# Kernel tuning notes

Measured on AMD Instinct MI355X. Metric: run time of the kernel, lower is better.

Reference implementation:

```python
import jax, jax.numpy as jnp
import numpy as np

B, T_ENC, IN, H, SEQ_OUT = 1024, 50, 99, 2112, 25


def _lstm_cell(x, h, c, W_ih, b_ih, W_hh, b_hh):
    # gates: [B, 4H], torch LSTMCell gate order is i, f, g, o
    gates = x @ W_ih.T + b_ih + h @ W_hh.T + b_hh
    i, f, g, o = jnp.split(gates, 4, axis=-1)
    c_new = jax.nn.sigmoid(f) * c + jax.nn.sigmoid(i) * jnp.tanh(g)
    h_new = jax.nn.sigmoid(o) * jnp.tanh(c_new)
    return h_new, c_new


def setup_inputs() -> dict:
    key = jax.random.key(0)
    ks = jax.random.split(key, 14)
    s = 0.04
    return {
        "hidden_states": jax.random.normal(ks[0], (B, T_ENC, H), jnp.float32),
        "cell_states": jax.random.normal(ks[1], (B, T_ENC, H), jnp.float32),
        "global_t_state": jax.random.normal(ks[2], (B, H), jnp.float32),
        "p": jax.random.normal(ks[3], (B, 1, IN), jnp.float32),
        "W_ih0": jax.random.normal(ks[4], (4 * H, IN), jnp.float32) * s,
        "b_ih0": jax.random.normal(ks[5], (4 * H,), jnp.float32) * s,
        "W_hh0": jax.random.normal(ks[6], (4 * H, H), jnp.float32) * s,
        "b_hh0": jax.random.normal(ks[7], (4 * H,), jnp.float32) * s,
        "W_ih1": jax.random.normal(ks[8], (4 * H, H), jnp.float32) * s,
        "b_ih1": jax.random.normal(ks[9], (4 * H,), jnp.float32) * s,
        "W_hh1": jax.random.normal(ks[10], (4 * H, H), jnp.float32) * s,
        "b_hh1": jax.random.normal(ks[11], (4 * H,), jnp.float32) * s,
        "W_out": jax.random.normal(ks[12], (H, IN), jnp.float32) * s,
        "b_out": jax.random.normal(ks[13], (IN,), jnp.float32) * s,
    }


def reference(hidden_states, cell_states, global_t_state, p,
              W_ih0, b_ih0, W_hh0, b_hh0,
              W_ih1, b_ih1, W_hh1, b_hh1,
              W_out, b_out):
    # initial states: layer 0 uses mean over encoder hidden states,
    # layer 1 uses mean over [global_t_state ; hidden_states]
    h0 = hidden_states.mean(axis=1)                                   # [B, H]
    h1 = jnp.concatenate((global_t_state[:, None, :], hidden_states), axis=1).mean(axis=1)
    c0 = cell_states.mean(axis=1)
    c1 = c0
    pre0 = p[:, 0, :]                                                 # seed input [B, IN]

    def step(carry, _):
        h0, c0, h1, c1, prev = carry
        h0n, c0n = _lstm_cell(prev, h0, c0, W_ih0, b_ih0, W_hh0, b_hh0)
        h1n, c1n = _lstm_cell(h0n, h1, c1, W_ih1, b_ih1, W_hh1, b_hh1)
        pre = h1n @ W_out + b_out + prev                              # residual on cell-0 input
        return (h0n, c0n, h1n, c1n, pre), pre

    _, pres = jax.lax.scan(step, (h0, c0, h1, c1, pre0), None, length=SEQ_OUT)
    return pres.transpose(1, 0, 2)                                    # [B, SEQ_OUT, IN]
```

## Files before the change

kernel.cpp:

```cpp
#include <hip/hip_runtime.h>

#define B_    1024
#define H_    2112
#define FH    8448
#define IN_   99
#define TENC  50
#define SEQ   25
#define K0    2240
#define K1    4224
#define LDX0  2240
#define LDX1  4224
#define KT0   35
#define KT1   66
#define HB_   132

typedef __bf16 bf16;
typedef __bf16 bf16x8 __attribute__((ext_vector_type(8)));
typedef __bf16 bf16x4 __attribute__((ext_vector_type(4)));
typedef float  f32x4  __attribute__((ext_vector_type(4)));

__device__ __forceinline__ void gload_lds16(const void* g, void* l) {
  __builtin_amdgcn_global_load_lds(
      (const __attribute__((address_space(1))) void*)g,
      (__attribute__((address_space(3))) void*)l, 16, 0, 0);
}

__device__ __forceinline__ float sigf(float x) { return 1.f / (1.f + __expf(-x)); }
__device__ __forceinline__ float tanhfast(float x) { return 1.f - 2.f / (__expf(2.f * x) + 1.f); }

__global__ __launch_bounds__(128, 3)
void lstm_gemm_cell(const bf16* __restrict__ X, int lda, int K,
                    const bf16* __restrict__ Wpk,
                    const float* __restrict__ bsum,
                    float* __restrict__ Cst,
                    bf16* __restrict__ d1, int ld1,
                    bf16* __restrict__ d2, int ld2)
{
  __shared__ __align__(16) bf16 As[128 * 64];

  const int vid = (blockIdx.x & 7) * 132 + (blockIdx.x >> 3);
  const int hb  = vid >> 3;
  const int hc0 = hb * 16;
  const int m0  = (vid & 7) * 128;

  const int tid  = threadIdx.x;
  const int srow = tid >> 3;
  const int scol = ((tid & 7) ^ (srow & 7)) * 8;

  const bf16* Ab = X + (size_t)(m0 + srow) * lda + scol;

  const int lane = tid & 63;
  const int w    = tid >> 6;
  const int lr   = lane & 15, lq = lane >> 4;
  const int xs   = lr & 7;
  const int cof0 = (lq ^ xs) * 8;
  const int cof1 = ((4 + lq) ^ xs) * 8;

  const int KT = K >> 6;
  const bf16* Wp = Wpk + (size_t)hb * KT * 4096 + lane * 8;

  f32x4 acc[4][4];
#pragma unroll
  for (int a = 0; a < 4; ++a)
#pragma unroll
    for (int b = 0; b < 4; ++b) acc[a][b] = (f32x4){0.f, 0.f, 0.f, 0.f};

  for (int kt = 0; kt < KT; ++kt) {
    const int ko = kt * 64;
#pragma unroll
    for (int it = 0; it < 8; ++it)
      gload_lds16(Ab + (size_t)it * 16 * lda + ko, &As[it * 1024 + tid * 8]);

    const bf16* Wt = Wp + (size_t)kt * 4096;
    bf16x8 bfr[4][2];
#pragma unroll
    for (int nf = 0; nf < 4; ++nf) {
      bfr[nf][0] = *(const bf16x8*)&Wt[(nf * 2 + 0) * 512];
      bfr[nf][1] = *(const bf16x8*)&Wt[(nf * 2 + 1) * 512];
    }
    __syncthreads();

    bf16x8 af[4][2];
#pragma unroll
    for (int mi = 0; mi < 4; ++mi) {
      const int r = (w * 64 + mi * 16 + lr) * 64;
      af[mi][0] = *(const bf16x8*)&As[r + cof0];
      af[mi][1] = *(const bf16x8*)&As[r + cof1];
    }
#pragma unroll
    for (int mi = 0; mi < 4; ++mi)
#pragma unroll
      for (int nf = 0; nf < 4; ++nf)
#pragma unroll
        for (int kc = 0; kc < 2; ++kc)
          acc[mi][nf] = __builtin_amdgcn_mfma_f32_16x16x32_bf16(
              af[mi][kc], bfr[nf][kc], acc[mi][nf], 0, 0, 0);
    __syncthreads();
  }

  const int hc = hc0 + lr;
  const float bi  = bsum[hc];
  const float bff = bsum[H_ + hc];
  const float bg  = bsum[2 * H_ + hc];
  const float bo  = bsum[3 * H_ + hc];

#pragma unroll
  for (int mi = 0; mi < 4; ++mi) {
#pragma unroll
    for (int r = 0; r < 4; ++r) {
      const int m = m0 + w * 64 + mi * 16 + lq * 4 + r;
      const float gi = acc[mi][0][r] + bi;
      const float gf = acc[mi][1][r] + bff;
      const float gg = acc[mi][2][r] + bg;
      const float go = acc[mi][3][r] + bo;
      const size_t ci = (size_t)m * H_ + hc;
      const float c_old = Cst[ci];
      const float cn = sigf(gf) * c_old + sigf(gi) * tanhfast(gg);
      const float hn = sigf(go) * tanhfast(cn);
      Cst[ci] = cn;
      const bf16 hb2 = (bf16)hn;
      d1[(size_t)m * ld1 + hc] = hb2;
      if (d2) d2[(size_t)m * ld2 + hc] = hb2;
    }
  }
}

__global__ __launch_bounds__(256, 1)
void out_gemm(const bf16* __restrict__ Hin,
              const bf16* __restrict__ Wo,
              const float* __restrict__ b_out,
              float* __restrict__ prev,
              bf16* __restrict__ X0n,
              float* __restrict__ out, int t)
{
  __shared__ float red[4][4][112];
  const int tid = threadIdx.x;
  const int m0 = blockIdx.x * 4;
  const int lane = tid & 63, wv = tid >> 6;
  const int lr = lane & 15, lq = lane >> 4, lk = lq * 8;

  f32x4 acc[7];
#pragma unroll
  for (int b = 0; b < 7; ++b) acc[b] = (f32x4){0.f, 0.f, 0.f, 0.f};

  const int start = (wv == 0) ? 0 : (1 + wv * 8);
  const int cnt = (wv == 0) ? 9 : 8;

  for (int kt = start; kt < start + cnt; ++kt) {
    const int ko = kt * 64;
    bf16x8 av[2], bv[7][2];
#pragma unroll
    for (int kc = 0; kc < 2; ++kc)
      av[kc] = *(const bf16x8*)&Hin[(size_t)(m0 + (lr & 3)) * LDX1 + ko + kc * 32 + lk];
#pragma unroll
    for (int nf = 0; nf < 7; ++nf)
#pragma unroll
      for (int kc = 0; kc < 2; ++kc)
        bv[nf][kc] = *(const bf16x8*)&Wo[(size_t)(nf * 16 + lr) * H_ + ko + kc * 32 + lk];
#pragma unroll
    for (int nf = 0; nf < 7; ++nf)
#pragma unroll
      for (int kc = 0; kc < 2; ++kc)
        acc[nf] = __builtin_amdgcn_mfma_f32_16x16x32_bf16(av[kc], bv[nf][kc], acc[nf], 0, 0, 0);
  }

  if (lq == 0) {
#pragma unroll
    for (int nf = 0; nf < 7; ++nf)
#pragma unroll
      for (int r = 0; r < 4; ++r)
        red[wv][r][nf * 16 + lr] = acc[nf][r];
  }
  __syncthreads();

  for (int idx = tid; idx < 4 * 112; idx += 256) {
    const int ml = idx / 112, n = idx - ml * 112;
    if (n < IN_) {
      const int m = m0 + ml;
      float s = red[0][ml][n] + red[1][ml][n] + red[2][ml][n] + red[3][ml][n] + b_out[n];
      const float pre = s + prev[m * 112 + n];
      prev[m * 112 + n] = pre;
      out[((size_t)m * SEQ + t) * IN_ + n] = pre;
      X0n[(size_t)m * LDX0 + n] = (bf16)pre;
    }
  }
}

__global__ void init_state(const float* __restrict__ hs, const float* __restrict__ cs,
                           const float* __restrict__ gts,
                           bf16* __restrict__ X0a, bf16* __restrict__ X1a,
                           float* __restrict__ c0, float* __restrict__ c1)
{
  const int h4 = blockIdx.x * 256 + threadIdx.x;
  if (h4 >= 528) return;
  const int b = blockIdx.y;
  const float4* hp = (const float4*)(hs + (size_t)b * TENC * H_) + h4;
  const float4* cp = (const float4*)(cs + (size_t)b * TENC * H_) + h4;
  float4 sh = {0.f, 0.f, 0.f, 0.f}, sc = {0.f, 0.f, 0.f, 0.f};
  for (int tt = 0; tt < TENC; ++tt) {
    float4 a = hp[tt * 528];
    sh.x += a.x; sh.y += a.y; sh.z += a.z; sh.w += a.w;
    float4 c = cp[tt * 528];
    sc.x += c.x; sc.y += c.y; sc.z += c.z; sc.w += c.w;
  }
  const float4 g = ((const float4*)(gts + (size_t)b * H_))[h4];
  const float4 c0v = {sc.x / 50.f, sc.y / 50.f, sc.z / 50.f, sc.w / 50.f};
  ((float4*)(c0 + (size_t)b * H_))[h4] = c0v;
  ((float4*)(c1 + (size_t)b * H_))[h4] = c0v;
  bf16x4 h0b = {(bf16)(sh.x / 50.f), (bf16)(sh.y / 50.f), (bf16)(sh.z / 50.f), (bf16)(sh.w / 50.f)};
  *(bf16x4*)&X0a[(size_t)b * LDX0 + 128 + h4 * 4] = h0b;
  bf16x4 h1b = {(bf16)((sh.x + g.x) / 51.f), (bf16)((sh.y + g.y) / 51.f),
                (bf16)((sh.z + g.z) / 51.f), (bf16)((sh.w + g.w) / 51.f)};
  *(bf16x4*)&X1a[(size_t)b * LDX1 + 2112 + h4 * 4] = h1b;
}

__global__ void init_prev(const float* __restrict__ p, float* __restrict__ prev,
                          bf16* __restrict__ X0a, bf16* __restrict__ X0b)
{
  const int idx = blockIdx.x * 256 + threadIdx.x;
  const int b = idx >> 7, n = idx & 127;
  const float v = (n < IN_) ? p[(size_t)b * IN_ + n] : 0.f;
  if (n < 112) prev[b * 112 + n] = v;
  X0a[(size_t)b * LDX0 + n] = (bf16)v;
  X0b[(size_t)b * LDX0 + n] = (bf16)0.f;
}

__global__ void pack_w0_frag(const float* __restrict__ Wih, const float* __restrict__ Whh,
                             bf16* __restrict__ Wpk)
{
  const int kt = blockIdx.x, hb = blockIdx.y;
  const int lane = threadIdx.x;
  const int lr = lane & 15, lq = lane >> 4;
  bf16* dst = Wpk + (((size_t)hb * KT0 + kt) * 8) * 512 + lane * 8;
#pragma unroll
  for (int fi = 0; fi < 8; ++fi) {
    const int nf = fi >> 1, kc = fi & 1;
    const int row = nf * H_ + hb * 16 + lr;
    const int k0 = kt * 64 + kc * 32 + lq * 8;
    bf16x8 v;
#pragma unroll
    for (int e = 0; e < 8; ++e) {
      const int k = k0 + e;
      float f;
      if (k < IN_)        f = Wih[(size_t)row * IN_ + k];
      else if (k < 128)   f = 0.f;
      else                f = Whh[(size_t)row * H_ + (k - 128)];
      v[e] = (bf16)f;
    }
    *(bf16x8*)(dst + fi * 512) = v;
  }
}

__global__ void pack_w1_frag(const float* __restrict__ Wih, const float* __restrict__ Whh,
                             bf16* __restrict__ Wpk)
{
  const int kt = blockIdx.x, hb = blockIdx.y;
  const int lane = threadIdx.x;
  const int lr = lane & 15, lq = lane >> 4;
  bf16* dst = Wpk + (((size_t)hb * KT1 + kt) * 8) * 512 + lane * 8;
#pragma unroll
  for (int fi = 0; fi < 8; ++fi) {
    const int nf = fi >> 1, kc = fi & 1;
    const int row = nf * H_ + hb * 16 + lr;
    const int k0 = kt * 64 + kc * 32 + lq * 8;
    bf16x8 v;
#pragma unroll
    for (int e = 0; e < 8; ++e) {
      const int k = k0 + e;
      const float f = (k < H_) ? Wih[(size_t)row * H_ + k]
                               : Whh[(size_t)row * H_ + (k - H_)];
      v[e] = (bf16)f;
    }
    *(bf16x8*)(dst + fi * 512) = v;
  }
}

__global__ void pack_wo(const float* __restrict__ W, bf16* __restrict__ Wo)
{
  const int n = blockIdx.x;
  for (int k = threadIdx.x; k < H_; k += 256)
    Wo[(size_t)n * H_ + k] = (n < IN_) ? (bf16)W[(size_t)k * IN_ + n] : (bf16)0.f;
}

__global__ void pack_bias(const float* __restrict__ bi0, const float* __restrict__ bh0,
                          const float* __restrict__ bi1, const float* __restrict__ bh1,
                          float* __restrict__ bs0, float* __restrict__ bs1)
{
  const int i = blockIdx.x * 256 + threadIdx.x;
  if (i < FH) { bs0[i] = bi0[i] + bh0[i]; bs1[i] = bi1[i] + bh1[i]; }
}

extern "C" void kernel_launch(void* const* d_in, const int* in_sizes, int n_in,
                              void* d_out, int out_size, void* d_ws, size_t ws_size,
                              hipStream_t stream)
{
  (void)in_sizes; (void)n_in; (void)out_size; (void)ws_size;
  const float* hs   = (const float*)d_in[0];
  const float* cs   = (const float*)d_in[1];
  const float* gts  = (const float*)d_in[2];
  const float* p    = (const float*)d_in[3];
  const float* Wih0 = (const float*)d_in[4];
  const float* bih0 = (const float*)d_in[5];
  const float* Whh0 = (const float*)d_in[6];
  const float* bhh0 = (const float*)d_in[7];
  const float* Wih1 = (const float*)d_in[8];
  const float* bih1 = (const float*)d_in[9];
  const float* Whh1 = (const float*)d_in[10];
  const float* bhh1 = (const float*)d_in[11];
  const float* Wout = (const float*)d_in[12];
  const float* bout = (const float*)d_in[13];
  float* out = (float*)d_out;

  char* ws = (char*)d_ws;
  size_t off = 0;
  auto alloc = [&](size_t bytes) -> void* {
    void* q = ws + off; off += (bytes + 255) & ~(size_t)255; return q;
  };
  bf16* Wc0 = (bf16*)alloc((size_t)HB_ * KT0 * 4096 * 2);
  bf16* Wc1 = (bf16*)alloc((size_t)HB_ * KT1 * 4096 * 2);
  bf16* Wo  = (bf16*)alloc((size_t)112 * H_ * 2);
  float* bs0 = (float*)alloc((size_t)FH * 4);
  float* bs1 = (float*)alloc((size_t)FH * 4);
  bf16* X0[2] = {(bf16*)alloc((size_t)B_ * LDX0 * 2), (bf16*)alloc((size_t)B_ * LDX0 * 2)};
  bf16* X1[2] = {(bf16*)alloc((size_t)B_ * LDX1 * 2), (bf16*)alloc((size_t)B_ * LDX1 * 2)};
  float* c0  = (float*)alloc((size_t)B_ * H_ * 4);
  float* c1  = (float*)alloc((size_t)B_ * H_ * 4);
  float* prev = (float*)alloc((size_t)B_ * 112 * 4);

  pack_w0_frag<<<dim3(KT0, HB_), 64, 0, stream>>>(Wih0, Whh0, Wc0);
  pack_w1_frag<<<dim3(KT1, HB_), 64, 0, stream>>>(Wih1, Whh1, Wc1);
  pack_wo<<<112, 256, 0, stream>>>(Wout, Wo);
  pack_bias<<<(FH + 255) / 256, 256, 0, stream>>>(bih0, bhh0, bih1, bhh1, bs0, bs1);
  init_prev<<<(B_ * 128) / 256, 256, 0, stream>>>(p, prev, X0[0], X0[1]);
  init_state<<<dim3(3, B_), 256, 0, stream>>>(hs, cs, gts, X0[0], X1[0], c0, c1);

  for (int t = 0; t < SEQ; ++t) {
    const int cur = t & 1, nxt = cur ^ 1;
    lstm_gemm_cell<<<1056, 128, 0, stream>>>(
        X0[cur], LDX0, K0, Wc0, bs0, c0, X1[cur], LDX1, X0[nxt] + 128, LDX0);
    lstm_gemm_cell<<<1056, 128, 0, stream>>>(
        X1[cur], LDX1, K1, Wc1, bs1, c1, X1[nxt] + 2112, LDX1, (bf16*)nullptr, 0);
    out_gemm<<<256, 256, 0, stream>>>(X1[nxt] + 2112, Wo, bout, prev, X0[nxt], out, t);
  }
}
```

Baseline: 5.012 ms.

## Widen LSTM GEMM tile to 32 hidden columns and double-buffer LDS

The LSTM gate GEMM block now covers 128 rows by 32 hidden columns (4 gates each) using 4 waves in a 2x2 arrangement, so each A tile staged in LDS is reused across twice as many output columns. The K loop is double-buffered with two LDS tiles and two register sets of B fragments, so the next tile's global loads overlap the current tile's MFMAs. The weight packing kernels are changed to the new 32-column fragment layout. The intent is to halve A-operand traffic and hide load latency, at the cost of half as many blocks, more LDS per block and higher register pressure.

```diff
diff --git a/kernel.cpp b/kernel.cpp
--- a/kernel.cpp
+++ b/kernel.cpp
@@ -12,7 +12,7 @@
 #define LDX1  4224
 #define KT0   35
 #define KT1   66
-#define HB_   132
+#define HB32  66
 
 typedef __bf16 bf16;
 typedef __bf16 bf16x8 __attribute__((ext_vector_type(8)));
@@ -28,7 +28,7 @@
 __device__ __forceinline__ float sigf(float x) { return 1.f / (1.f + __expf(-x)); }
 __device__ __forceinline__ float tanhfast(float x) { return 1.f - 2.f / (__expf(2.f * x) + 1.f); }
 
-__global__ __launch_bounds__(128, 3)
+__global__ __launch_bounds__(256, 2)
 void lstm_gemm_cell(const bf16* __restrict__ X, int lda, int K,
                     const bf16* __restrict__ Wpk,
                     const float* __restrict__ bsum,
@@ -36,11 +36,12 @@
                     bf16* __restrict__ d1, int ld1,
                     bf16* __restrict__ d2, int ld2)
 {
-  __shared__ __align__(16) bf16 As[128 * 64];
-
-  const int vid = (blockIdx.x & 7) * 132 + (blockIdx.x >> 3);
+  __shared__ __align__(16) bf16 As0[128 * 64];
+  __shared__ __align__(16) bf16 As1[128 * 64];
+
+  const int vid = (blockIdx.x & 7) * 66 + (blockIdx.x >> 3);
   const int hb  = vid >> 3;
-  const int hc0 = hb * 16;
+  const int hc0 = hb * 32;
   const int m0  = (vid & 7) * 128;
 
   const int tid  = threadIdx.x;
@@ -50,14 +51,15 @@
   const bf16* Ab = X + (size_t)(m0 + srow) * lda + scol;
 
   const int lane = tid & 63;
-  const int w    = tid >> 6;
-  const int lr   = lane & 15, lq = lane >> 4;
-  const int xs   = lr & 7;
+  const int wv = tid >> 6;
+  const int wm = wv >> 1, wn = wv & 1;
+  const int lr = lane & 15, lq = lane >> 4;
+  const int xs = lr & 7;
   const int cof0 = (lq ^ xs) * 8;
   const int cof1 = ((4 + lq) ^ xs) * 8;
 
   const int KT = K >> 6;
-  const bf16* Wp = Wpk + (size_t)hb * KT * 4096 + lane * 8;
+  const bf16* Wp = Wpk + (((size_t)hb * KT) * 16 + wn * 8) * 512 + lane * 8;
 
   f32x4 acc[4][4];
 #pragma unroll
@@ -65,40 +67,61 @@
 #pragma unroll
     for (int b = 0; b < 4; ++b) acc[a][b] = (f32x4){0.f, 0.f, 0.f, 0.f};
 
-  for (int kt = 0; kt < KT; ++kt) {
-    const int ko = kt * 64;
-#pragma unroll
-    for (int it = 0; it < 8; ++it)
-      gload_lds16(Ab + (size_t)it * 16 * lda + ko, &As[it * 1024 + tid * 8]);
-
-    const bf16* Wt = Wp + (size_t)kt * 4096;
-    bf16x8 bfr[4][2];
-#pragma unroll
-    for (int nf = 0; nf < 4; ++nf) {
-      bfr[nf][0] = *(const bf16x8*)&Wt[(nf * 2 + 0) * 512];
-      bfr[nf][1] = *(const bf16x8*)&Wt[(nf * 2 + 1) * 512];
-    }
+#define STAGE(kt, AD) do {                                                   \
+    const int ko_ = (kt) * 64;                                               \
+    _Pragma("unroll")                                                        \
+    for (int it = 0; it < 4; ++it)                                           \
+      gload_lds16(Ab + (size_t)(it * 32) * lda + ko_, &AD[it * 2048 + tid * 8]); \
+  } while (0)
+
+#define LOADB(BR, kt) do {                                                   \
+    const bf16* Wt_ = Wp + (size_t)(kt) * (16 * 512);                        \
+    _Pragma("unroll")                                                        \
+    for (int fi = 0; fi < 8; ++fi)                                           \
+      BR[fi] = *(const bf16x8*)&Wt_[fi * 512];                               \
+  } while (0)
+
+#define COMPUTE(AS, BR) do {                                                 \
+    bf16x8 af_[4][2];                                                        \
+    _Pragma("unroll")                                                        \
+    for (int mi = 0; mi < 4; ++mi) {                                         \
+      const int r_ = (wm * 64 + mi * 16 + lr) * 64;                          \
+      af_[mi][0] = *(const bf16x8*)&AS[r_ + cof0];                           \
+      af_[mi][1] = *(const bf16x8*)&AS[r_ + cof1];                           \
+    }                                                                        \
+    _Pragma("unroll")                                                        \
+    for (int mi = 0; mi < 4; ++mi)                                           \
+      _Pragma("unroll")                                                      \
+      for (int nf = 0; nf < 4; ++nf) {                                       \
+        acc[mi][nf] = __builtin_amdgcn_mfma_f32_16x16x32_bf16(               \
+            af_[mi][0], BR[nf * 2 + 0], acc[mi][nf], 0, 0, 0);               \
+        acc[mi][nf] = __builtin_amdgcn_mfma_f32_16x16x32_bf16(               \
+            af_[mi][1], BR[nf * 2 + 1], acc[mi][nf], 0, 0, 0);               \
+      }                                                                      \
+  } while (0)
+
+  bf16x8 bA[8], bB[8];
+  LOADB(bA, 0);
+  STAGE(0, As0);
+  __syncthreads();
+
+  int kt = 0;
+  for (; kt + 2 <= KT; kt += 2) {
+    LOADB(bB, kt + 1);
+    STAGE(kt + 1, As1);
+    COMPUTE(As0, bA);
     __syncthreads();
-
-    bf16x8 af[4][2];
-#pragma unroll
-    for (int mi = 0; mi < 4; ++mi) {
-      const int r = (w * 64 + mi * 16 + lr) * 64;
-      af[mi][0] = *(const bf16x8*)&As[r + cof0];
-      af[mi][1] = *(const bf16x8*)&As[r + cof1];
-    }
-#pragma unroll
-    for (int mi = 0; mi < 4; ++mi)
-#pragma unroll
-      for (int nf = 0; nf < 4; ++nf)
-#pragma unroll
-        for (int kc = 0; kc < 2; ++kc)
-          acc[mi][nf] = __builtin_amdgcn_mfma_f32_16x16x32_bf16(
-              af[mi][kc], bfr[nf][kc], acc[mi][nf], 0, 0, 0);
+    if (kt + 2 < KT) { LOADB(bA, kt + 2); STAGE(kt + 2, As0); }
+    COMPUTE(As1, bB);
     __syncthreads();
   }
-
-  const int hc = hc0 + lr;
+  if (KT & 1)
+    COMPUTE(As0, bA);
+#undef COMPUTE
+#undef LOADB
+#undef STAGE
+
+  const int hc = hc0 + wn * 16 + lr;
   const float bi  = bsum[hc];
   const float bff = bsum[H_ + hc];
   const float bg  = bsum[2 * H_ + hc];
@@ -108,7 +131,7 @@
   for (int mi = 0; mi < 4; ++mi) {
 #pragma unroll
     for (int r = 0; r < 4; ++r) {
-      const int m = m0 + w * 64 + mi * 16 + lq * 4 + r;
+      const int m = m0 + wm * 64 + mi * 16 + lq * 4 + r;
       const float gi = acc[mi][0][r] + bi;
       const float gf = acc[mi][1][r] + bff;
       const float gg = acc[mi][2][r] + bg;
@@ -229,22 +252,22 @@
                              bf16* __restrict__ Wpk)
 {
   const int kt = blockIdx.x, hb = blockIdx.y;
-  const int lane = threadIdx.x;
+  const int wn = threadIdx.x >> 6, lane = threadIdx.x & 63;
   const int lr = lane & 15, lq = lane >> 4;
-  bf16* dst = Wpk + (((size_t)hb * KT0 + kt) * 8) * 512 + lane * 8;
+  bf16* dst = Wpk + (((size_t)hb * KT0 + kt) * 16 + wn * 8) * 512 + lane * 8;
 #pragma unroll
   for (int fi = 0; fi < 8; ++fi) {
     const int nf = fi >> 1, kc = fi & 1;
-    const int row = nf * H_ + hb * 16 + lr;
+    const int row = nf * H_ + hb * 32 + wn * 16 + lr;
     const int k0 = kt * 64 + kc * 32 + lq * 8;
     bf16x8 v;
 #pragma unroll
     for (int e = 0; e < 8; ++e) {
       const int k = k0 + e;
       float f;
-      if (k < IN_)        f = Wih[(size_t)row * IN_ + k];
-      else if (k < 128)   f = 0.f;
-      else                f = Whh[(size_t)row * H_ + (k - 128)];
+      if (k < IN_)      f = Wih[(size_t)row * IN_ + k];
+      else if (k < 128) f = 0.f;
+      else              f = Whh[(size_t)row * H_ + (k - 128)];
       v[e] = (bf16)f;
     }
     *(bf16x8*)(dst + fi * 512) = v;
@@ -255,13 +278,13 @@
                              bf16* __restrict__ Wpk)
 {
   const int kt = blockIdx.x, hb = blockIdx.y;
-  const int lane = threadIdx.x;
+  const int wn = threadIdx.x >> 6, lane = threadIdx.x & 63;
   const int lr = lane & 15, lq = lane >> 4;
-  bf16* dst = Wpk + (((size_t)hb * KT1 + kt) * 8) * 512 + lane * 8;
+  bf16* dst = Wpk + (((size_t)hb * KT1 + kt) * 16 + wn * 8) * 512 + lane * 8;
 #pragma unroll
   for (int fi = 0; fi < 8; ++fi) {
     const int nf = fi >> 1, kc = fi & 1;
-    const int row = nf * H_ + hb * 16 + lr;
+    const int row = nf * H_ + hb * 32 + wn * 16 + lr;
     const int k0 = kt * 64 + kc * 32 + lq * 8;
     bf16x8 v;
 #pragma unroll
@@ -316,8 +339,8 @@
   auto alloc = [&](size_t bytes) -> void* {
     void* q = ws + off; off += (bytes + 255) & ~(size_t)255; return q;
   };
-  bf16* Wc0 = (bf16*)alloc((size_t)HB_ * KT0 * 4096 * 2);
-  bf16* Wc1 = (bf16*)alloc((size_t)HB_ * KT1 * 4096 * 2);
+  bf16* Wc0 = (bf16*)alloc((size_t)HB32 * KT0 * 16 * 512 * 2);
+  bf16* Wc1 = (bf16*)alloc((size_t)HB32 * KT1 * 16 * 512 * 2);
   bf16* Wo  = (bf16*)alloc((size_t)112 * H_ * 2);
   float* bs0 = (float*)alloc((size_t)FH * 4);
   float* bs1 = (float*)alloc((size_t)FH * 4);
@@ -327,8 +350,8 @@
   float* c1  = (float*)alloc((size_t)B_ * H_ * 4);
   float* prev = (float*)alloc((size_t)B_ * 112 * 4);
 
-  pack_w0_frag<<<dim3(KT0, HB_), 64, 0, stream>>>(Wih0, Whh0, Wc0);
-  pack_w1_frag<<<dim3(KT1, HB_), 64, 0, stream>>>(Wih1, Whh1, Wc1);
+  pack_w0_frag<<<dim3(KT0, HB32), 128, 0, stream>>>(Wih0, Whh0, Wc0);
+  pack_w1_frag<<<dim3(KT1, HB32), 128, 0, stream>>>(Wih1, Whh1, Wc1);
   pack_wo<<<112, 256, 0, stream>>>(Wout, Wo);
   pack_bias<<<(FH + 255) / 256, 256, 0, stream>>>(bih0, bhh0, bih1, bhh1, bs0, bs1);
   init_prev<<<(B_ * 128) / 256, 256, 0, stream>>>(p, prev, X0[0], X0[1]);
@@ -336,9 +359,9 @@
 
   for (int t = 0; t < SEQ; ++t) {
     const int cur = t & 1, nxt = cur ^ 1;
-    lstm_gemm_cell<<<1056, 128, 0, stream>>>(
+    lstm_gemm_cell<<<528, 256, 0, stream>>>(
         X0[cur], LDX0, K0, Wc0, bs0, c0, X1[cur], LDX1, X0[nxt] + 128, LDX0);
-    lstm_gemm_cell<<<1056, 128, 0, stream>>>(
+    lstm_gemm_cell<<<528, 256, 0, stream>>>(
         X1[cur], LDX1, K1, Wc1, bs1, c1, X1[nxt] + 2112, LDX1, (bf16*)nullptr, 0);
     out_gemm<<<256, 256, 0, stream>>>(X1[nxt] + 2112, Wo, bout, prev, X0[nxt], out, t);
   }
```

Measured after the change: 5.764 ms. 15.0% more time.
